# Kernel optimization log

Hardware: AMD Instinct MI355X
Metric: run time of the kernel (lower is better)

The kernel has to match this reference:

```python
import jax, jax.numpy as jnp
import numpy as np

B, T, I, H, O = 128, 512, 128, 256, 1

def setup_inputs() -> dict:
    key = jax.random.key(0)
    ks = jax.random.split(key, 7)
    s_ih = 1.0 / np.sqrt(H)
    return {
        "x": jax.random.normal(ks[0], (B, T, I), dtype=jnp.float32),
        "W_ih": jax.random.uniform(ks[1], (H, I), minval=-s_ih, maxval=s_ih, dtype=jnp.float32),
        "W_hh": jax.random.uniform(ks[2], (H, H), minval=-s_ih, maxval=s_ih, dtype=jnp.float32),
        "b_ih": jax.random.uniform(ks[3], (H,), minval=-s_ih, maxval=s_ih, dtype=jnp.float32),
        "b_hh": jax.random.uniform(ks[4], (H,), minval=-s_ih, maxval=s_ih, dtype=jnp.float32),
        "W_fc": jax.random.uniform(ks[5], (O, H), minval=-s_ih, maxval=s_ih, dtype=jnp.float32),
        "b_fc": jax.random.uniform(ks[6], (O,), minval=-s_ih, maxval=s_ih, dtype=jnp.float32),
    }

def reference(x, W_ih, W_hh, b_ih, b_hh, W_fc, b_fc):
    # Precompute input projections for all timesteps: [B, T, H]
    xp = jnp.einsum("bti,hi->bth", x, W_ih) + b_ih + b_hh
    h0 = jnp.zeros((x.shape[0], W_hh.shape[0]), dtype=x.dtype)

    def step(h, xp_t):
        h_new = jnp.tanh(xp_t + h @ W_hh.T)
        return h_new, None

    # scan over time axis; only final hidden state is needed
    h_last, _ = jax.lax.scan(step, h0, jnp.swapaxes(xp, 0, 1))
    logits = h_last @ W_fc.T + b_fc
    return jax.nn.sigmoid(logits)
```

## Files before the change

### kernel.cpp

```cpp
#include <hip/hip_runtime.h>
#include <hip/hip_bf16.h>


#define B_ 128
#define T_ 512
#define I_ 128
#define H_ 256
#define BB 8
#define SCALE 2.8853900817779268f
#define WSC 2032.0f
#define HSC 127.0f
#define WHS (WSC * HSC)
#define SCOMB (SCALE / WHS)
#define MAGICQ 12583039.0f

typedef __attribute__((ext_vector_type(8))) short short8;
typedef __attribute__((ext_vector_type(4))) float floatx4;
typedef __attribute__((ext_vector_type(4))) int int4v;

__device__ __forceinline__ short8 pack8(float4 lo, float4 hi) {
    __hip_bfloat162 p0 = __float22bfloat162_rn(float2{lo.x, lo.y});
    __hip_bfloat162 p1 = __float22bfloat162_rn(float2{lo.z, lo.w});
    __hip_bfloat162 p2 = __float22bfloat162_rn(float2{hi.x, hi.y});
    __hip_bfloat162 p3 = __float22bfloat162_rn(float2{hi.z, hi.w});
    int4 i;
    i.x = *(int*)&p0; i.y = *(int*)&p1; i.z = *(int*)&p2; i.w = *(int*)&p3;
    return *(short8*)&i;
}
__device__ __forceinline__ int q4(float a, float b, float c, float d, float s) {
    int qa = (int)rintf(a * s) & 255;
    int qb = (int)rintf(b * s) & 255;
    int qc = (int)rintf(c * s) & 255;
    int qd = (int)rintf(d * s) & 255;
    return qa | (qb << 8) | (qc << 16) | (qd << 24);
}
__device__ __forceinline__ float tq(int acci) {
    float v = (float)acci * SCOMB;
    float e = __builtin_amdgcn_exp2f(v);
    float rc = __builtin_amdgcn_rcpf(e + 1.0f);
    return __builtin_fmaf(-254.0f, rc, MAGICQ);
}

#define XP_GRID 256
#define XP_NT   ((B_ * T_ / 16) / XP_GRID)
__global__ __launch_bounds__(256, 1)
void xp_kernel(const float* __restrict__ x, const float* __restrict__ W_ih,
               const float* __restrict__ b_ih, const float* __restrict__ b_hh,
               int* __restrict__ xq) {
    const int tid  = threadIdx.x;
    const int wave = tid >> 6, lane = tid & 63;
    const int l15  = lane & 15, quad = lane >> 4;
    const int n0   = wave * 64;

    short8 wfrag[4][4];
#pragma unroll
    for (int mtt = 0; mtt < 4; ++mtt)
#pragma unroll
        for (int kq = 0; kq < 4; ++kq) {
            const float* p = W_ih + (long)(n0 + mtt * 16 + l15) * I_ + kq * 32 + quad * 8;
            wfrag[mtt][kq] = pack8(*(const float4*)p, *(const float4*)(p + 4));
        }
    floatx4 biasv[4];
#pragma unroll
    for (int mtt = 0; mtt < 4; ++mtt)
#pragma unroll
        for (int r = 0; r < 4; ++r) {
            int n = n0 + mtt * 16 + quad * 4 + r;
            biasv[mtt][r] = b_ih[n] + b_hh[n];
        }

    const long mbase = (long)blockIdx.x * XP_NT * 16;

    float4 qa[4][2], qb[4][2];
#define LDX(Q, IT)                                                              \
    {                                                                           \
        const int itc = ((IT) < XP_NT) ? (IT) : (XP_NT - 1);                    \
        const float* p = x + (mbase + (long)itc * 16 + l15) * I_ + quad * 8;    \
        _Pragma("unroll")                                                       \
        for (int kq = 0; kq < 4; ++kq) {                                        \
            Q[kq][0] = *(const float4*)(p + kq * 32);                           \
            Q[kq][1] = *(const float4*)(p + kq * 32 + 4);                       \
        }                                                                       \
    }
#define ITER(Q, IT, ILD)                                                        \
    {                                                                           \
        short8 xf[4];                                                           \
        _Pragma("unroll")                                                       \
        for (int kq = 0; kq < 4; ++kq) xf[kq] = pack8(Q[kq][0], Q[kq][1]);      \
        LDX(Q, ILD);                                                            \
        floatx4 acc[4];                                                         \
        _Pragma("unroll")                                                       \
        for (int mtt = 0; mtt < 4; ++mtt) acc[mtt] = biasv[mtt];                \
        _Pragma("unroll")                                                       \
        for (int kq = 0; kq < 4; ++kq)                                          \
            _Pragma("unroll")                                                   \
            for (int mtt = 0; mtt < 4; ++mtt)                                   \
                acc[mtt] = __builtin_amdgcn_mfma_f32_16x16x32_bf16(             \
                    wfrag[mtt][kq], xf[kq], acc[mtt], 0, 0, 0);                 \
        int* o = xq + (mbase + (long)(IT) * 16 + l15) * H_ + n0 + quad * 4;     \
        _Pragma("unroll")                                                       \
        for (int mtt = 0; mtt < 4; ++mtt) {                                     \
            int4 st;                                                            \
            st.x = (int)rintf(acc[mtt][0] * WHS);                               \
            st.y = (int)rintf(acc[mtt][1] * WHS);                               \
            st.z = (int)rintf(acc[mtt][2] * WHS);                               \
            st.w = (int)rintf(acc[mtt][3] * WHS);                               \
            *(int4*)(o + mtt * 16) = st;                                        \
        }                                                                       \
    }

    LDX(qa, 0);
    LDX(qb, 1);
#pragma unroll 1
    for (int it = 0; it < XP_NT; it += 2) {
        ITER(qa, it, it + 2);
        ITER(qb, it + 1, it + 3);
    }
#undef ITER
#undef LDX
}

__global__ __launch_bounds__(512, 2)
void rnn_kernel(const int* __restrict__ xq, const float* __restrict__ W_hh,
                const float* __restrict__ W_fc, const float* __restrict__ b_fc,
                float* __restrict__ out) {
    __shared__ __align__(16) signed char hbuf[2][16][256];
    const int tid  = threadIdx.x;
    const int wave = tid >> 6, lane = tid & 63;
    const int l15  = lane & 15, quad = lane >> 4;
    const int b0   = blockIdx.x * BB;
    const int n0   = wave * 32;
    const int swz  = l15 & 7;

    int4v wfrag[2][4];
#pragma unroll
    for (int mt = 0; mt < 2; ++mt)
#pragma unroll
        for (int kq = 0; kq < 4; ++kq) {
            const float* p = W_hh + (long)(n0 + mt * 16 + l15) * H_ + kq * 64 + quad * 16;
            int4v f;
#pragma unroll
            for (int j = 0; j < 4; ++j) {
                float4 w = *(const float4*)(p + j * 4);
                f[j] = q4(w.x, w.y, w.z, w.w, WSC);
            }
            wfrag[mt][kq] = f;
        }

    {
        int* hz = (int*)&hbuf[0][0][0];
        for (int i = tid; i < 2 * 16 * 256 / 4; i += 512) hz[i] = 0;
    }

    int roff[4];
#pragma unroll
    for (int kq = 0; kq < 4; ++kq)
        roff[kq] = l15 * 256 + (((kq * 4 + quad) ^ swz) << 4);
    int woff[2];
#pragma unroll
    for (int mt = 0; mt < 2; ++mt) {
        int c = wave * 2 + mt;
        woff[mt] = l15 * 256 + ((c ^ swz) << 4) + quad * 4;
    }

    const int bcl = (l15 < BB) ? l15 : (BB - 1);
    const int* xql = xq + (long)(b0 + bcl) * T_ * H_ + n0 + quad * 4;
    int4v xvA0 = *(const int4v*)(xql);
    int4v xvA1 = *(const int4v*)(xql + 16);
    int4v xvB0 = *(const int4v*)(xql + H_);
    int4v xvB1 = *(const int4v*)(xql + H_ + 16);

    __syncthreads();

    const signed char* hb0r = &hbuf[0][0][0]; signed char* hb0w = &hbuf[0][0][0];
    const signed char* hb1r = &hbuf[1][0][0]; signed char* hb1w = &hbuf[1][0][0];

#define BAR() asm volatile("s_waitcnt lgkmcnt(0)\n\ts_barrier" ::: "memory")

#define STEP(HR, HW, XV0, XV1, TLD)                                             \
    {                                                                           \
                      \
        int4v hfrag[4];                                                         \
        _Pragma("unroll")                                                       \
        for (int kq = 0; kq < 4; ++kq)                                          \
            hfrag[kq] = *(const int4v*)((HR) + roff[kq]);                       \
                           \
        int4v aC[2], aZ[2];                                                     \
        aC[0] = XV0; aC[1] = XV1;                                               \
        aZ[0] = (int4v){0, 0, 0, 0};                                            \
        aZ[1] = (int4v){0, 0, 0, 0};                                            \
        XV0 = *(const int4v*)(xql + (long)(TLD) * H_);                          \
        XV1 = *(const int4v*)(xql + (long)(TLD) * H_ + 16);                     \
               \
        _Pragma("unroll")                                                       \
        for (int kq = 0; kq < 2; ++kq)                                          \
            _Pragma("unroll")                                                   \
            for (int mt = 0; mt < 2; ++mt) {                                    \
                aC[mt] = __builtin_amdgcn_mfma_i32_16x16x64_i8(                 \
                    wfrag[mt][kq], hfrag[kq], aC[mt], 0, 0, 0);                 \
                aZ[mt] = __builtin_amdgcn_mfma_i32_16x16x64_i8(                 \
                    wfrag[mt][kq + 2], hfrag[kq + 2], aZ[mt], 0, 0, 0);         \
            }                                                                   \
             \
        if (l15 < BB) {                                                         \
            _Pragma("unroll")                                                   \
            for (int mt = 0; mt < 2; ++mt) {                                    \
                float f0 = tq(aC[mt][0] + aZ[mt][0]);                           \
                float f1 = tq(aC[mt][1] + aZ[mt][1]);                           \
                float f2 = tq(aC[mt][2] + aZ[mt][2]);                           \
                float f3 = tq(aC[mt][3] + aZ[mt][3]);                           \
                unsigned t01 = __builtin_amdgcn_perm(                           \
                    *(unsigned*)&f1, *(unsigned*)&f0, 0x00000400u);             \
                unsigned t23 = __builtin_amdgcn_perm(                           \
                    *(unsigned*)&f3, *(unsigned*)&f2, 0x00000400u);             \
                unsigned pk  = __builtin_amdgcn_perm(t23, t01, 0x05040100u);    \
                *(int*)((HW) + woff[mt]) = (int)pk;                             \
            }                                                                   \
        }                                                                       \
        BAR();                                                                  \
    }

#pragma unroll 1
    for (int t = 0; t < T_; t += 2) {
        const int tl0 = (t + 2 < T_) ? t + 2 : T_ - 1;
        const int tl1 = (t + 3 < T_) ? t + 3 : T_ - 1;
        STEP(hb0r, hb1w, xvA0, xvA1, tl0);
        STEP(hb1r, hb0w, xvB0, xvB1, tl1);
    }
#undef STEP
#undef BAR

    if (tid < BB * 16) {
        const int bl = tid >> 4, seg = tid & 15;
        const int bswz = bl & 7;
        const signed char* hr = &hbuf[0][0][0] + bl * 256 + ((seg ^ bswz) << 4);
        float p = 0.0f;
#pragma unroll
        for (int i = 0; i < 16; ++i)
            p += (float)hr[i] * W_fc[seg * 16 + i];
#pragma unroll
        for (int off = 1; off < 16; off <<= 1) p += __shfl_xor(p, off);
        if (seg == 0)
            out[b0 + bl] = 1.0f / (1.0f + __expf(-(p * (1.0f / HSC) + b_fc[0])));
    }
}

extern "C" void kernel_launch(void* const* d_in, const int* in_sizes, int n_in,
                              void* d_out, int out_size, void* d_ws, size_t ws_size,
                              hipStream_t stream) {
    const float* x    = (const float*)d_in[0];
    const float* W_ih = (const float*)d_in[1];
    const float* W_hh = (const float*)d_in[2];
    const float* b_ih = (const float*)d_in[3];
    const float* b_hh = (const float*)d_in[4];
    const float* W_fc = (const float*)d_in[5];
    const float* b_fc = (const float*)d_in[6];
    float* out = (float*)d_out;

    int* xq = (int*)d_ws;

    xp_kernel<<<XP_GRID, 256, 0, stream>>>(x, W_ih, b_ih, b_hh, xq);
    rnn_kernel<<<B_ / BB, 512, 0, stream>>>(xq, W_hh, W_fc, b_fc, out);
}
```

Baseline: 333.2 us.

## Use 16 batch rows per block with 4 waves each owning 64 hidden units

The RNN kernel now handles 16 batch rows per block (all 16 MFMA columns used) with 256 threads, and each wave computes 64 hidden outputs instead of 32. This halves the grid to 8 blocks and removes the wasted half of each MFMA tile and the per-lane batch guard. Each wave holds twice the weight fragments and prefetched input registers, and the per-step barrier covers fewer waves. In exchange, each wave issues more serial MFMAs per timestep on the critical path, and only 8 CUs are used.

```diff
diff --git a/kernel.cpp b/kernel.cpp
--- a/kernel.cpp
+++ b/kernel.cpp
@@ -6,7 +6,6 @@
 #define T_ 512
 #define I_ 128
 #define H_ 256
-#define BB 8
 #define SCALE 2.8853900817779268f
 #define WSC 2032.0f
 #define HSC 127.0f
@@ -120,7 +119,7 @@
 #undef LDX
 }
 
-__global__ __launch_bounds__(512, 2)
+__global__ __launch_bounds__(256, 1)
 void rnn_kernel(const int* __restrict__ xq, const float* __restrict__ W_hh,
                 const float* __restrict__ W_fc, const float* __restrict__ b_fc,
                 float* __restrict__ out) {
@@ -128,13 +127,13 @@
     const int tid  = threadIdx.x;
     const int wave = tid >> 6, lane = tid & 63;
     const int l15  = lane & 15, quad = lane >> 4;
-    const int b0   = blockIdx.x * BB;
-    const int n0   = wave * 32;
+    const int b0   = blockIdx.x * 16;
+    const int n0   = wave * 64;
     const int swz  = l15 & 7;
 
-    int4v wfrag[2][4];
-#pragma unroll
-    for (int mt = 0; mt < 2; ++mt)
+    int4v wfrag[4][4];
+#pragma unroll
+    for (int mt = 0; mt < 4; ++mt)
 #pragma unroll
         for (int kq = 0; kq < 4; ++kq) {
             const float* p = W_hh + (long)(n0 + mt * 16 + l15) * H_ + kq * 64 + quad * 16;
@@ -149,26 +148,27 @@
 
     {
         int* hz = (int*)&hbuf[0][0][0];
-        for (int i = tid; i < 2 * 16 * 256 / 4; i += 512) hz[i] = 0;
+        for (int i = tid; i < 2 * 16 * 256 / 4; i += 256) hz[i] = 0;
     }
 
     int roff[4];
 #pragma unroll
     for (int kq = 0; kq < 4; ++kq)
         roff[kq] = l15 * 256 + (((kq * 4 + quad) ^ swz) << 4);
-    int woff[2];
-#pragma unroll
-    for (int mt = 0; mt < 2; ++mt) {
-        int c = wave * 2 + mt;
+    int woff[4];
+#pragma unroll
+    for (int mt = 0; mt < 4; ++mt) {
+        int c = wave * 4 + mt;
         woff[mt] = l15 * 256 + ((c ^ swz) << 4) + quad * 4;
     }
 
-    const int bcl = (l15 < BB) ? l15 : (BB - 1);
-    const int* xql = xq + (long)(b0 + bcl) * T_ * H_ + n0 + quad * 4;
-    int4v xvA0 = *(const int4v*)(xql);
-    int4v xvA1 = *(const int4v*)(xql + 16);
-    int4v xvB0 = *(const int4v*)(xql + H_);
-    int4v xvB1 = *(const int4v*)(xql + H_ + 16);
+    const int* xql = xq + (long)(b0 + l15) * T_ * H_ + n0 + quad * 4;
+    int4v xv[2][4];
+#pragma unroll
+    for (int mt = 0; mt < 4; ++mt) {
+        xv[0][mt] = *(const int4v*)(xql + mt * 16);
+        xv[1][mt] = *(const int4v*)(xql + H_ + mt * 16);
+    }
 
     __syncthreads();
 
@@ -177,45 +177,46 @@
 
 #define BAR() asm volatile("s_waitcnt lgkmcnt(0)\n\ts_barrier" ::: "memory")
 
-#define STEP(HR, HW, XV0, XV1, TLD)                                             \
+#define STEP(HR, HW, P, TLD)                                                    \
     {                                                                           \
                       \
         int4v hfrag[4];                                                         \
         _Pragma("unroll")                                                       \
         for (int kq = 0; kq < 4; ++kq)                                          \
             hfrag[kq] = *(const int4v*)((HR) + roff[kq]);                       \
-                           \
-        int4v aC[2], aZ[2];                                                     \
-        aC[0] = XV0; aC[1] = XV1;                                               \
-        aZ[0] = (int4v){0, 0, 0, 0};                                            \
-        aZ[1] = (int4v){0, 0, 0, 0};                                            \
-        XV0 = *(const int4v*)(xql + (long)(TLD) * H_);                          \
-        XV1 = *(const int4v*)(xql + (long)(TLD) * H_ + 16);                     \
-               \
+                        \
+        int4v aC[4], aZ[4];                                                     \
+        _Pragma("unroll")                                                       \
+        for (int mt = 0; mt < 4; ++mt) {                                        \
+            aC[mt] = xv[P][mt];                                                 \
+            aZ[mt] = (int4v){0, 0, 0, 0};                                       \
+        }                                                                       \
+        _Pragma("unroll")                                                       \
+        for (int mt = 0; mt < 4; ++mt)                                          \
+            xv[P][mt] = *(const int4v*)(xql + (long)(TLD) * H_ + mt * 16);      \
+              \
         _Pragma("unroll")                                                       \
         for (int kq = 0; kq < 2; ++kq)                                          \
             _Pragma("unroll")                                                   \
-            for (int mt = 0; mt < 2; ++mt) {                                    \
+            for (int mt = 0; mt < 4; ++mt) {                                    \
                 aC[mt] = __builtin_amdgcn_mfma_i32_16x16x64_i8(                 \
                     wfrag[mt][kq], hfrag[kq], aC[mt], 0, 0, 0);                 \
                 aZ[mt] = __builtin_amdgcn_mfma_i32_16x16x64_i8(                 \
                     wfrag[mt][kq + 2], hfrag[kq + 2], aZ[mt], 0, 0, 0);         \
             }                                                                   \
              \
-        if (l15 < BB) {                                                         \
-            _Pragma("unroll")                                                   \
-            for (int mt = 0; mt < 2; ++mt) {                                    \
-                float f0 = tq(aC[mt][0] + aZ[mt][0]);                           \
-                float f1 = tq(aC[mt][1] + aZ[mt][1]);                           \
-                float f2 = tq(aC[mt][2] + aZ[mt][2]);                           \
-                float f3 = tq(aC[mt][3] + aZ[mt][3]);                           \
-                unsigned t01 = __builtin_amdgcn_perm(                           \
-                    *(unsigned*)&f1, *(unsigned*)&f0, 0x00000400u);             \
-                unsigned t23 = __builtin_amdgcn_perm(                           \
-                    *(unsigned*)&f3, *(unsigned*)&f2, 0x00000400u);             \
-                unsigned pk  = __builtin_amdgcn_perm(t23, t01, 0x05040100u);    \
-                *(int*)((HW) + woff[mt]) = (int)pk;                             \
-            }                                                                   \
+        _Pragma("unroll")                                                       \
+        for (int mt = 0; mt < 4; ++mt) {                                        \
+            float f0 = tq(aC[mt][0] + aZ[mt][0]);                               \
+            float f1 = tq(aC[mt][1] + aZ[mt][1]);                               \
+            float f2 = tq(aC[mt][2] + aZ[mt][2]);                               \
+            float f3 = tq(aC[mt][3] + aZ[mt][3]);                               \
+            unsigned t01 = __builtin_amdgcn_perm(                               \
+                *(unsigned*)&f1, *(unsigned*)&f0, 0x00000400u);                 \
+            unsigned t23 = __builtin_amdgcn_perm(                               \
+                *(unsigned*)&f3, *(unsigned*)&f2, 0x00000400u);                 \
+            unsigned pk  = __builtin_amdgcn_perm(t23, t01, 0x05040100u);        \
+            *(int*)((HW) + woff[mt]) = (int)pk;                                 \
         }                                                                       \
         BAR();                                                                  \
     }
@@ -224,13 +225,13 @@
     for (int t = 0; t < T_; t += 2) {
         const int tl0 = (t + 2 < T_) ? t + 2 : T_ - 1;
         const int tl1 = (t + 3 < T_) ? t + 3 : T_ - 1;
-        STEP(hb0r, hb1w, xvA0, xvA1, tl0);
-        STEP(hb1r, hb0w, xvB0, xvB1, tl1);
+        STEP(hb0r, hb1w, 0, tl0);
+        STEP(hb1r, hb0w, 1, tl1);
     }
 #undef STEP
 #undef BAR
 
-    if (tid < BB * 16) {
+    {
         const int bl = tid >> 4, seg = tid & 15;
         const int bswz = bl & 7;
         const signed char* hr = &hbuf[0][0][0] + bl * 256 + ((seg ^ bswz) << 4);
@@ -260,5 +261,5 @@
     int* xq = (int*)d_ws;
 
     xp_kernel<<<XP_GRID, 256, 0, stream>>>(x, W_ih, b_ih, b_hh, xq);
-    rnn_kernel<<<B_ / BB, 512, 0, stream>>>(xq, W_hh, W_fc, b_fc, out);
-}
+    rnn_kernel<<<B_ / 16, 256, 0, stream>>>(xq, W_hh, W_fc, b_fc, out);
+}
```

Result: slower. 443.9 us (+33.2%).
